# Optimization experiments

Hardware: AMD Instinct MI355X
Metric: run time of the kernel (lower is better)

Reference implementation:

```python
import jax, jax.numpy as jnp
import numpy as np

N_NODES = 100000
N_EDGES = 1600000
IN_DIM = 128
HID = 64
N_CLASSES = 40
NEG_SLOPE = 0.2


def setup_inputs() -> dict:
    key = jax.random.key(0)
    ks = jax.random.split(key, 12)
    s_in = 1.0 / np.sqrt(IN_DIM)
    s_h = 1.0 / np.sqrt(HID)
    return {
        "x": jax.random.normal(ks[0], (N_NODES, IN_DIM), dtype=jnp.float32),
        "edge_index": jax.random.randint(ks[1], (2, N_EDGES), 0, N_NODES, dtype=jnp.int64),
        "W0": jax.random.normal(ks[2], (IN_DIM, HID), dtype=jnp.float32) * s_in,
        "a_s0": jax.random.normal(ks[3], (HID,), dtype=jnp.float32) * s_h,
        "a_d0": jax.random.normal(ks[4], (HID,), dtype=jnp.float32) * s_h,
        "b0": jnp.zeros((HID,), dtype=jnp.float32),
        "W1": jax.random.normal(ks[5], (HID, HID), dtype=jnp.float32) * s_h,
        "a_s1": jax.random.normal(ks[6], (HID,), dtype=jnp.float32) * s_h,
        "a_d1": jax.random.normal(ks[7], (HID,), dtype=jnp.float32) * s_h,
        "b1": jnp.zeros((HID,), dtype=jnp.float32),
        "Wl": jax.random.normal(ks[8], (HID, N_CLASSES), dtype=jnp.float32) * s_h,
        "bl": jnp.zeros((N_CLASSES,), dtype=jnp.float32),
    }


def gat_conv(x, src, dst, W, a_s, a_d, b, n_nodes):
    # single-head GATConv (PyG default heads=1), self-loops already in src/dst
    h = x @ W                                  # [N, d]
    e = jax.nn.leaky_relu((h @ a_s)[src] + (h @ a_d)[dst], NEG_SLOPE)  # [E]
    # segment softmax over incoming edges of each dst node
    m = jax.ops.segment_max(e, dst, num_segments=n_nodes)
    p = jnp.exp(e - m[dst])
    denom = jax.ops.segment_sum(p, dst, num_segments=n_nodes)
    alpha = p / (denom[dst] + 1e-16)           # [E]
    out = jax.ops.segment_sum(alpha[:, None] * h[src], dst, num_segments=n_nodes)
    return out + b


def reference(x, edge_index, W0, a_s0, a_d0, b0, W1, a_s1, a_d1, b1, Wl, bl):
    n = x.shape[0]
    loop = jnp.arange(n, dtype=edge_index.dtype)
    src = jnp.concatenate([edge_index[0], loop])
    dst = jnp.concatenate([edge_index[1], loop])
    h = gat_conv(x, src, dst, W0, a_s0, a_d0, b0, n)
    h = jax.nn.elu(h)
    h = gat_conv(h, src, dst, W1, a_s1, a_d1, b1, n)
    h = jax.nn.elu(h)
    return h @ Wl + bl
```

## Files before the change

kernel.cpp:

```cpp
#include <hip/hip_runtime.h>
#include <math.h>

#define NEG_SLOPE 0.2f
#define CAP 256
#define BSH 9
#define BSZ 512
#define CHUNK 8192

typedef __attribute__((ext_vector_type(8))) short short8;
typedef __attribute__((ext_vector_type(4))) float f32x4;

__device__ __forceinline__ float hred_sum(float v) {
#pragma unroll
    for (int o = 16; o >= 1; o >>= 1) v += __shfl_xor(v, o, 64);
    return v;
}
__device__ __forceinline__ unsigned int f2bf(float f) {
    unsigned int u = __float_as_uint(f);
    return (u + 0x7fffu + ((u >> 16) & 1u)) >> 16;
}
__device__ __forceinline__ float bflo(unsigned int u) { return __uint_as_float(u << 16); }
__device__ __forceinline__ float bfhi(unsigned int u) { return __uint_as_float(u & 0xffff0000u); }


__global__ __launch_bounds__(256) void k_zero(int* p, int n) {
    int i = blockIdx.x * 256 + threadIdx.x;
    if (i < n) p[i] = 0;
}

__global__ __launch_bounds__(256) void k_hist(const int* __restrict__ dst, int* __restrict__ bcount, int E) {
    __shared__ int lh[256];
    lh[threadIdx.x] = 0;
    __syncthreads();
    int stride = gridDim.x * 256;
    for (int i = blockIdx.x * 256 + threadIdx.x; i < E; i += stride)
        atomicAdd(&lh[dst[i] >> BSH], 1);
    __syncthreads();
    int c = lh[threadIdx.x];
    if (c) atomicAdd(&bcount[threadIdx.x], c);
}

__global__ __launch_bounds__(256) void k_bscan(const int* __restrict__ bcount,
                                               int* __restrict__ eoff, int* __restrict__ boff,
                                               int* __restrict__ bcursor, int* __restrict__ rowptr,
                                               int nbuck, int N, int E) {
    __shared__ int s1[256], s2[256];
    int t = threadIdx.x;
    int bc = (t < nbuck) ? bcount[t] : 0;
    int cn = 0;
    if (t < nbuck) { cn = N - (t << BSH); if (cn > BSZ) cn = BSZ; if (cn < 0) cn = 0; }
    int tot = bc + cn;
    s1[t] = bc; s2[t] = tot;
    __syncthreads();
#pragma unroll
    for (int off = 1; off < 256; off <<= 1) {
        int u1 = (t >= off) ? s1[t - off] : 0;
        int u2 = (t >= off) ? s2[t - off] : 0;
        __syncthreads();
        s1[t] += u1; s2[t] += u2;
        __syncthreads();
    }
    if (t < nbuck) {
        int e = s1[t] - bc, b = s2[t] - tot;
        eoff[t] = e; boff[t] = b; bcursor[t] = e;
    }
    if (t == 0) rowptr[N] = E + N;
}

__global__ __launch_bounds__(256) void k_scatter(const int* __restrict__ src, const int* __restrict__ dst,
                                                 int* __restrict__ bcursor, int* __restrict__ ebuf, int E) {
    __shared__ int lh[256], lb[256];
    int base = blockIdx.x * CHUNK;
    int end = base + CHUNK; if (end > E) end = E;
    lh[threadIdx.x] = 0;
    __syncthreads();
    for (int i = base + threadIdx.x; i < end; i += 256)
        atomicAdd(&lh[dst[i] >> BSH], 1);
    __syncthreads();
    int c = lh[threadIdx.x];
    lb[threadIdx.x] = c ? atomicAdd(&bcursor[threadIdx.x], c) : 0;
    lh[threadIdx.x] = 0;
    __syncthreads();
    for (int i = base + threadIdx.x; i < end; i += 256) {
        int d = dst[i], b = d >> BSH;
        int p = atomicAdd(&lh[b], 1);
        ebuf[lb[b] + p] = (src[i] << BSH) | (d & (BSZ - 1));
    }
}

__global__ __launch_bounds__(512) void k_build(const int* __restrict__ eoff, const int* __restrict__ boff,
                                               const int* __restrict__ bcount, const int* __restrict__ ebuf,
                                               int* __restrict__ rowptr, int* __restrict__ csr, int N) {
    __shared__ int sdeg[BSZ], sscan[BSZ];
    int b = blockIdx.x, t = threadIdx.x;
    int nlo = b << BSH;
    int cn = N - nlo; if (cn > BSZ) cn = BSZ;
    int e0 = eoff[b], ec = bcount[b], cb = boff[b];
    sdeg[t] = (t < cn) ? 1 : 0;
    __syncthreads();
    for (int i = t; i < ec; i += 512)
        atomicAdd(&sdeg[ebuf[e0 + i] & (BSZ - 1)], 1);
    __syncthreads();
    int v = sdeg[t];
    sscan[t] = v;
    __syncthreads();
#pragma unroll
    for (int off = 1; off < BSZ; off <<= 1) {
        int u = (t >= off) ? sscan[t - off] : 0;
        __syncthreads();
        sscan[t] += u;
        __syncthreads();
    }
    int excl = sscan[t] - v;
    if (t < cn) {
        rowptr[nlo + t] = cb + excl;
        csr[cb + excl] = nlo + t;
        sdeg[t] = excl + 1;
    }
    __syncthreads();
    for (int i = t; i < ec; i += 512) {
        int rec = ebuf[e0 + i];
        int p = atomicAdd(&sdeg[rec & (BSZ - 1)], 1);
        csr[cb + p] = rec >> BSH;
    }
}


template <int K, int OUTW, bool SS, bool HB>
__global__ __launch_bounds__(256) void k_gemm(const float* __restrict__ X,
                                              const float* __restrict__ W,
                                              const float* __restrict__ a_s,
                                              const float* __restrict__ a_d,
                                              const float* __restrict__ bias,
                                              void* __restrict__ Hout,
                                              float* __restrict__ ss,
                                              float* __restrict__ sd, int N) {
    constexpr int NKC = K / 32;
    constexpr int NC  = (OUTW + 15) / 16;
    __shared__ __align__(16) short wfrag[NKC * NC * 64 * 8];
    __shared__ __align__(16) unsigned int hs[HB ? 4 : 1][16 * 32];

    const int tid  = threadIdx.x;
    const int lane = tid & 63;
    const int w    = tid >> 6;
    const int m    = lane & 15;
    const int q8   = lane >> 4;
    const int rowbase = blockIdx.x * 64 + w * 16;

    for (int f = tid; f < NKC * NC * 64; f += 256) {
        int flane = f & 63;
        int fc    = (f >> 6) % NC;
        int fkc   = (f >> 6) / NC;
        int col   = fc * 16 + (flane & 15);
        int k0    = fkc * 32 + (flane >> 4) * 8;
        short8 b;
#pragma unroll
        for (int j = 0; j < 8; ++j) {
            float v = (col < OUTW) ? W[(k0 + j) * OUTW + col] : 0.f;
            b[j] = (short)f2bf(v);
        }
        *(short8*)&wfrag[f * 8] = b;
    }
    __syncthreads();

    int grow = rowbase + m; if (grow >= N) grow = N - 1;
    const float* xrow = X + (size_t)grow * K + q8 * 8;

    f32x4 acc[NC];
#pragma unroll
    for (int c = 0; c < NC; ++c) acc[c] = (f32x4)0.f;

#pragma unroll
    for (int kc = 0; kc < NKC; ++kc) {
        float4 v0 = *(const float4*)(xrow + kc * 32);
        float4 v1 = *(const float4*)(xrow + kc * 32 + 4);
        float vv[8] = {v0.x, v0.y, v0.z, v0.w, v1.x, v1.y, v1.z, v1.w};
        short8 ah, al;
#pragma unroll
        for (int j = 0; j < 8; ++j) {
            unsigned int hb16 = f2bf(vv[j]);
            ah[j] = (short)hb16;
            al[j] = (short)f2bf(vv[j] - __uint_as_float(hb16 << 16));
        }
#pragma unroll
        for (int c = 0; c < NC; ++c) {
            short8 b = *(short8*)&wfrag[((kc * NC + c) * 64 + lane) * 8];
            acc[c] = __builtin_amdgcn_mfma_f32_16x16x32_bf16(ah, b, acc[c], 0, 0, 0);
            acc[c] = __builtin_amdgcn_mfma_f32_16x16x32_bf16(al, b, acc[c], 0, 0, 0);
        }
    }

    if (SS) {
        float asv[NC], adv[NC];
#pragma unroll
        for (int c = 0; c < NC; ++c) { asv[c] = a_s[c * 16 + m]; adv[c] = a_d[c * 16 + m]; }
#pragma unroll
        for (int i = 0; i < 4; ++i) {
            float s = 0.f, d = 0.f;
#pragma unroll
            for (int c = 0; c < NC; ++c) {
                s = fmaf(acc[c][i], asv[c], s);
                d = fmaf(acc[c][i], adv[c], d);
            }
#pragma unroll
            for (int o = 1; o <= 8; o <<= 1) {
                s += __shfl_xor(s, o, 64);
                d += __shfl_xor(d, o, 64);
            }
            int r = rowbase + q8 * 4 + i;
            if (m == 0 && r < N) { ss[r] = s; sd[r] = d; }
        }
    }

    if (HB) {
        unsigned short* hsw = (unsigned short*)&hs[w][0];
#pragma unroll
        for (int c = 0; c < NC; ++c)
#pragma unroll
            for (int i = 0; i < 4; ++i)
                hsw[(q8 * 4 + i) * 64 + c * 16 + m] = (unsigned short)f2bf(acc[c][i]);
        unsigned int* hu = &hs[w][0];
        int row = lane >> 2, u0 = (lane & 3) * 8;
        uint4 va = *(uint4*)&hu[row * 32 + u0];
        uint4 vb = *(uint4*)&hu[row * 32 + u0 + 4];
        int r = rowbase + row;
        if (r < N) {
            unsigned int* hbp = (unsigned int*)Hout;
            *(uint4*)&hbp[(size_t)r * 32 + u0]     = va;
            *(uint4*)&hbp[(size_t)r * 32 + u0 + 4] = vb;
        }
    } else {
        float bv[NC];
#pragma unroll
        for (int c = 0; c < NC; ++c) {
            int col = c * 16 + m;
            bv[c] = (col < OUTW) ? bias[col] : 0.f;
        }
        float* O = (float*)Hout;
#pragma unroll
        for (int i = 0; i < 4; ++i) {
            int r = rowbase + q8 * 4 + i;
            if (r < N) {
#pragma unroll
                for (int c = 0; c < NC; ++c) {
                    int col = c * 16 + m;
                    if (col < OUTW) O[(size_t)r * OUTW + col] = acc[c][i] + bv[c];
                }
            }
        }
    }
}


__global__ __launch_bounds__(256) void k_agg(const int* __restrict__ rowptr, const int* __restrict__ csr,
                                             const float* __restrict__ ss, const float* __restrict__ sd,
                                             const unsigned int* __restrict__ hb, const float* __restrict__ bias,
                                             float* __restrict__ z, int N) {
    __shared__ float2 ps[8 * CAP];
    const int tid = threadIdx.x;
    const int hw  = tid >> 5;
    const int p   = tid & 31;
    const int n   = blockIdx.x * 8 + hw;
    const bool valid = n < N;
    float2* myps = ps + hw * CAP;

    int ro = 0, deg = 0;
    float sdn = 0.f;
    if (valid) {
        ro  = rowptr[n];
        deg = rowptr[n + 1] - ro;
        sdn = sd[n];
    }

    if (deg <= CAP) {
        float sum = 0.f;
        for (int j = p; j < deg; j += 32) {
            int s = csr[ro + j];
            float e = ss[s] + sdn;
            e = fmaxf(e, NEG_SLOPE * e);
            float pe = __expf(e);
            myps[j] = make_float2(pe, __int_as_float(s));
            sum += pe;
        }
        sum = hred_sum(sum);
        float inv = 1.f / (sum + 1e-16f);

        float ax = 0.f, ay = 0.f, bx = 0.f, by = 0.f, cx = 0.f, cy = 0.f, dx = 0.f, dy = 0.f;
        int j = 0;
        for (; j + 3 < deg; j += 4) {
            float2 e0 = myps[j], e1 = myps[j + 1], e2 = myps[j + 2], e3 = myps[j + 3];
            unsigned int u0 = hb[(size_t)__float_as_int(e0.y) * 32 + p];
            unsigned int u1 = hb[(size_t)__float_as_int(e1.y) * 32 + p];
            unsigned int u2 = hb[(size_t)__float_as_int(e2.y) * 32 + p];
            unsigned int u3 = hb[(size_t)__float_as_int(e3.y) * 32 + p];
            ax = fmaf(bflo(u0), e0.x, ax); ay = fmaf(bfhi(u0), e0.x, ay);
            bx = fmaf(bflo(u1), e1.x, bx); by = fmaf(bfhi(u1), e1.x, by);
            cx = fmaf(bflo(u2), e2.x, cx); cy = fmaf(bfhi(u2), e2.x, cy);
            dx = fmaf(bflo(u3), e3.x, dx); dy = fmaf(bfhi(u3), e3.x, dy);
        }
        for (; j < deg; ++j) {
            float2 e0 = myps[j];
            unsigned int u0 = hb[(size_t)__float_as_int(e0.y) * 32 + p];
            ax = fmaf(bflo(u0), e0.x, ax); ay = fmaf(bfhi(u0), e0.x, ay);
        }
        float fx = (ax + bx) + (cx + dx);
        float fy = (ay + by) + (cy + dy);
        if (valid) {
            float2 ob = *(const float2*)&bias[p * 2];
            float ox = fmaf(fx, inv, ob.x);
            float oy = fmaf(fy, inv, ob.y);
            ox = (ox > 0.f) ? ox : __expf(ox) - 1.f;
            oy = (oy > 0.f) ? oy : __expf(oy) - 1.f;
            *(float2*)&z[(size_t)n * 64 + p * 2] = make_float2(ox, oy);
        }
    } else {
        float sum = 0.f;
        for (int j = p; j < deg; j += 32) {
            int s = csr[ro + j];
            float e = ss[s] + sdn;
            e = fmaxf(e, NEG_SLOPE * e);
            sum += __expf(e);
        }
        sum = hred_sum(sum);
        float inv = 1.f / (sum + 1e-16f);
        float fx = 0.f, fy = 0.f;
        for (int j = 0; j < deg; ++j) {
            int s = csr[ro + j];
            float e = ss[s] + sdn;
            e = fmaxf(e, NEG_SLOPE * e);
            float pe = __expf(e);
            unsigned int u = hb[(size_t)s * 32 + p];
            fx = fmaf(bflo(u), pe, fx); fy = fmaf(bfhi(u), pe, fy);
        }
        float2 ob = *(const float2*)&bias[p * 2];
        float ox = fmaf(fx, inv, ob.x);
        float oy = fmaf(fy, inv, ob.y);
        ox = (ox > 0.f) ? ox : __expf(ox) - 1.f;
        oy = (oy > 0.f) ? oy : __expf(oy) - 1.f;
        *(float2*)&z[(size_t)n * 64 + p * 2] = make_float2(ox, oy);
    }
}


extern "C" void kernel_launch(void* const* d_in, const int* in_sizes, int n_in,
                              void* d_out, int out_size, void* d_ws, size_t ws_size,
                              hipStream_t stream) {
    const float* x   = (const float*)d_in[0];
    const int*   ei  = (const int*)d_in[1];
    const float* W0  = (const float*)d_in[2];
    const float* as0 = (const float*)d_in[3];
    const float* ad0 = (const float*)d_in[4];
    const float* b0  = (const float*)d_in[5];
    const float* W1  = (const float*)d_in[6];
    const float* as1 = (const float*)d_in[7];
    const float* ad1 = (const float*)d_in[8];
    const float* b1  = (const float*)d_in[9];
    const float* Wl  = (const float*)d_in[10];
    const float* bl  = (const float*)d_in[11];
    float* out = (float*)d_out;

    int N = in_sizes[0] / 128;
    int E = in_sizes[1] / 2;
    const int* srcp = ei;
    const int* dstp = ei + E;
    int nbuck = (N + BSZ - 1) >> BSH;

    char* wp = (char*)d_ws;
    auto alloc = [&](size_t bytes) { void* p = (void*)wp; wp += (bytes + 255) & ~(size_t)255; return p; };
    unsigned int* hb = (unsigned int*)alloc((size_t)N * 32 * 4);
    float* z       = (float*)alloc((size_t)N * 64 * 4);
    float* ssb     = (float*)alloc((size_t)N * 4);
    float* sdb     = (float*)alloc((size_t)N * 4);
    int*   rowptr  = (int*)alloc((size_t)(N + 1) * 4);
    int*   csr     = (int*)alloc((size_t)(E + N) * 4);
    int*   ebuf    = (int*)alloc((size_t)E * 4);
    int*   bcount  = (int*)alloc(256 * 4);
    int*   eoff    = (int*)alloc(256 * 4);
    int*   boff    = (int*)alloc(256 * 4);
    int*   bcursor = (int*)alloc(256 * 4);

    k_zero<<<1, 256, 0, stream>>>(bcount, 256);
    k_hist<<<256, 256, 0, stream>>>(dstp, bcount, E);
    k_bscan<<<1, 256, 0, stream>>>(bcount, eoff, boff, bcursor, rowptr, nbuck, N, E);
    k_scatter<<<(E + CHUNK - 1) / CHUNK, 256, 0, stream>>>(srcp, dstp, bcursor, ebuf, E);
    k_build<<<nbuck, 512, 0, stream>>>(eoff, boff, bcount, ebuf, rowptr, csr, N);

    int gb = (N + 63) / 64;
    k_gemm<128, 64, true, true><<<gb, 256, 0, stream>>>(x, W0, as0, ad0, nullptr, hb, ssb, sdb, N);
    k_agg<<<(N + 7) / 8, 256, 0, stream>>>(rowptr, csr, ssb, sdb, hb, b0, z, N);
    k_gemm<64, 64, true, true><<<gb, 256, 0, stream>>>(z, W1, as1, ad1, nullptr, hb, ssb, sdb, N);
    k_agg<<<(N + 7) / 8, 256, 0, stream>>>(rowptr, csr, ssb, sdb, hb, b1, z, N);
    k_gemm<64, 40, false, false><<<gb, 256, 0, stream>>>(z, Wl, nullptr, nullptr, bl, out, nullptr, nullptr, N);
}
```

Measured before the change: 280.5 us.

## Pad bucket counters, shrink scatter chunk, precompute byte offsets in aggregation

```diff
diff --git a/kernel.cpp b/kernel.cpp
--- a/kernel.cpp
+++ b/kernel.cpp
@@ -5,7 +5,8 @@
 #define CAP 256
 #define BSH 9
 #define BSZ 512
-#define CHUNK 8192
+#define CHUNK 2048
+#define PADS 16
 
 typedef __attribute__((ext_vector_type(8))) short short8;
 typedef __attribute__((ext_vector_type(4))) float f32x4;
@@ -37,7 +38,7 @@
         atomicAdd(&lh[dst[i] >> BSH], 1);
     __syncthreads();
     int c = lh[threadIdx.x];
-    if (c) atomicAdd(&bcount[threadIdx.x], c);
+    if (c) atomicAdd(&bcount[threadIdx.x * PADS], c);
 }
 
 __global__ __launch_bounds__(256) void k_bscan(const int* __restrict__ bcount,
@@ -46,7 +47,7 @@
                                                int nbuck, int N, int E) {
     __shared__ int s1[256], s2[256];
     int t = threadIdx.x;
-    int bc = (t < nbuck) ? bcount[t] : 0;
+    int bc = (t < nbuck) ? bcount[t * PADS] : 0;
     int cn = 0;
     if (t < nbuck) { cn = N - (t << BSH); if (cn > BSZ) cn = BSZ; if (cn < 0) cn = 0; }
     int tot = bc + cn;
@@ -62,7 +63,7 @@
     }
     if (t < nbuck) {
         int e = s1[t] - bc, b = s2[t] - tot;
-        eoff[t] = e; boff[t] = b; bcursor[t] = e;
+        eoff[t] = e; boff[t] = b; bcursor[t * PADS] = e;
     }
     if (t == 0) rowptr[N] = E + N;
 }
@@ -78,7 +79,7 @@
         atomicAdd(&lh[dst[i] >> BSH], 1);
     __syncthreads();
     int c = lh[threadIdx.x];
-    lb[threadIdx.x] = c ? atomicAdd(&bcursor[threadIdx.x], c) : 0;
+    lb[threadIdx.x] = c ? atomicAdd(&bcursor[threadIdx.x * PADS], c) : 0;
     lh[threadIdx.x] = 0;
     __syncthreads();
     for (int i = base + threadIdx.x; i < end; i += 256) {
@@ -95,7 +96,7 @@
     int b = blockIdx.x, t = threadIdx.x;
     int nlo = b << BSH;
     int cn = N - nlo; if (cn > BSZ) cn = BSZ;
-    int e0 = eoff[b], ec = bcount[b], cb = boff[b];
+    int e0 = eoff[b], ec = bcount[b * PADS], cb = boff[b];
     sdeg[t] = (t < cn) ? 1 : 0;
     __syncthreads();
     for (int i = t; i < ec; i += 512)
@@ -263,6 +264,8 @@
     const int n   = blockIdx.x * 8 + hw;
     const bool valid = n < N;
     float2* myps = ps + hw * CAP;
+    const char* hbb = (const char*)hb;
+    const int p4 = p * 4;
 
     int ro = 0, deg = 0;
     float sdn = 0.f;
@@ -279,7 +282,7 @@
             float e = ss[s] + sdn;
             e = fmaxf(e, NEG_SLOPE * e);
             float pe = __expf(e);
-            myps[j] = make_float2(pe, __int_as_float(s));
+            myps[j] = make_float2(pe, __int_as_float((s << 7) + p4 - p4));
             sum += pe;
         }
         sum = hred_sum(sum);
@@ -289,10 +292,10 @@
         int j = 0;
         for (; j + 3 < deg; j += 4) {
             float2 e0 = myps[j], e1 = myps[j + 1], e2 = myps[j + 2], e3 = myps[j + 3];
-            unsigned int u0 = hb[(size_t)__float_as_int(e0.y) * 32 + p];
-            unsigned int u1 = hb[(size_t)__float_as_int(e1.y) * 32 + p];
-            unsigned int u2 = hb[(size_t)__float_as_int(e2.y) * 32 + p];
-            unsigned int u3 = hb[(size_t)__float_as_int(e3.y) * 32 + p];
+            unsigned int u0 = *(const unsigned int*)(hbb + (__float_as_int(e0.y) + p4));
+            unsigned int u1 = *(const unsigned int*)(hbb + (__float_as_int(e1.y) + p4));
+            unsigned int u2 = *(const unsigned int*)(hbb + (__float_as_int(e2.y) + p4));
+            unsigned int u3 = *(const unsigned int*)(hbb + (__float_as_int(e3.y) + p4));
             ax = fmaf(bflo(u0), e0.x, ax); ay = fmaf(bfhi(u0), e0.x, ay);
             bx = fmaf(bflo(u1), e1.x, bx); by = fmaf(bfhi(u1), e1.x, by);
             cx = fmaf(bflo(u2), e2.x, cx); cy = fmaf(bfhi(u2), e2.x, cy);
@@ -300,7 +303,7 @@
         }
         for (; j < deg; ++j) {
             float2 e0 = myps[j];
-            unsigned int u0 = hb[(size_t)__float_as_int(e0.y) * 32 + p];
+            unsigned int u0 = *(const unsigned int*)(hbb + (__float_as_int(e0.y) + p4));
             ax = fmaf(bflo(u0), e0.x, ax); ay = fmaf(bfhi(u0), e0.x, ay);
         }
         float fx = (ax + bx) + (cx + dx);
@@ -329,7 +332,7 @@
             float e = ss[s] + sdn;
             e = fmaxf(e, NEG_SLOPE * e);
             float pe = __expf(e);
-            unsigned int u = hb[(size_t)s * 32 + p];
+            unsigned int u = *(const unsigned int*)(hbb + ((s << 7) + p4));
             fx = fmaf(bflo(u), pe, fx); fy = fmaf(bfhi(u), pe, fy);
         }
         float2 ob = *(const float2*)&bias[p * 2];
@@ -374,12 +377,12 @@
     int*   rowptr  = (int*)alloc((size_t)(N + 1) * 4);
     int*   csr     = (int*)alloc((size_t)(E + N) * 4);
     int*   ebuf    = (int*)alloc((size_t)E * 4);
-    int*   bcount  = (int*)alloc(256 * 4);
+    int*   bcount  = (int*)alloc(256 * PADS * 4);
     int*   eoff    = (int*)alloc(256 * 4);
     int*   boff    = (int*)alloc(256 * 4);
-    int*   bcursor = (int*)alloc(256 * 4);
-
-    k_zero<<<1, 256, 0, stream>>>(bcount, 256);
+    int*   bcursor = (int*)alloc(256 * PADS * 4);
+
+    k_zero<<<(256 * PADS + 255) / 256, 256, 0, stream>>>(bcount, 256 * PADS);
     k_hist<<<256, 256, 0, stream>>>(dstp, bcount, E);
     k_bscan<<<1, 256, 0, stream>>>(bcount, eoff, boff, bcursor, rowptr, nbuck, N, E);
     k_scatter<<<(E + CHUNK - 1) / CHUNK, 256, 0, stream>>>(srcp, dstp, bcursor, ebuf, E);
```

Result: no change. 281.4 us (+0.3%).
